# Performance work log

Hardware: AMD Instinct MI355X
Metric: run time of the kernel (lower is better)

Reference implementation:

```python
import jax, jax.numpy as jnp
import numpy as np

B, T, C = 4, 2048, 2048  # batch, n_target, n_context
KEY_SIZE = 1024
VALUE_SIZE = 1024
NUM_HEADS = 16
KEY_HIDDEN = 64
HEAD_SIZE = VALUE_SIZE // NUM_HEADS  # 64
NORMALISE = True


def setup_inputs() -> dict:
    key = jax.random.key(0)
    ks = jax.random.split(key, 7)
    s = 0.02
    return {
        "queries": jax.random.normal(ks[0], (B, T, KEY_SIZE), jnp.float32),
        "keys": jax.random.normal(ks[1], (B, C, KEY_SIZE), jnp.float32),
        "values": jax.random.normal(ks[2], (B, C, VALUE_SIZE), jnp.float32),
        "Wq": jax.random.normal(ks[3], (NUM_HEADS * KEY_HIDDEN, KEY_SIZE), jnp.float32) * s,
        "Wk": jax.random.normal(ks[4], (NUM_HEADS * KEY_HIDDEN, KEY_SIZE), jnp.float32) * s,
        "Wv": jax.random.normal(ks[5], (NUM_HEADS * HEAD_SIZE, VALUE_SIZE), jnp.float32) * s,
        "Wo": jax.random.normal(ks[6], (VALUE_SIZE, NUM_HEADS * HEAD_SIZE), jnp.float32) * s,
    }


def reference(queries, keys, values, Wq, Wk, Wv, Wo):
    # Linear projections (torch nn.Linear: x @ W.T), reshape to heads
    q = (queries @ Wq.T).reshape(B, T, NUM_HEADS, KEY_HIDDEN)   # [B,T,H,Dk]
    k = (keys @ Wk.T).reshape(B, C, NUM_HEADS, KEY_HIDDEN)      # [B,C,H,Dk]
    v = (values @ Wv.T).reshape(B, C, NUM_HEADS, HEAD_SIZE)     # [B,C,H,Dv]
    scale = np.sqrt(KEY_HIDDEN).astype(np.float32)
    # Scores [B,H,T,C]
    scores = jnp.einsum('bthd,bchd->bhtc', q, k) / scale
    if NORMALISE:
        attn = jax.nn.softmax(scores, axis=-1)
    else:
        attn = jax.nn.sigmoid(scores)
    out = jnp.einsum('bhtc,bchd->bthd', attn, v)                # [B,T,H,Dv]
    out = out.reshape(B, T, NUM_HEADS * HEAD_SIZE)
    return out @ Wo.T                                            # [B,T,VALUE_SIZE]
```

## Files before the change

### kernel.cpp

```cpp
#include <hip/hip_runtime.h>
#include <stdint.h>

#define BATCH 4
#define SEQ   2048
#define EMB   1024
#define NH    16
#define HD    64

typedef __attribute__((ext_vector_type(4))) float  floatx4;
typedef __attribute__((ext_vector_type(8))) short  shortx8;

__device__ __forceinline__ unsigned short f2bf(float f) {
  unsigned u = __builtin_bit_cast(unsigned, f);
  u += 0x7FFFu + ((u >> 16) & 1u);
  return (unsigned short)(u >> 16);
}

__device__ __forceinline__ unsigned pack2bf(float a, float b) {
  return (unsigned)f2bf(a) | ((unsigned)f2bf(b) << 16);
}

__device__ __forceinline__ unsigned packtrunc(float a, float b) {
#if __has_builtin(__builtin_amdgcn_perm)
  return __builtin_amdgcn_perm(__builtin_bit_cast(unsigned, b),
                               __builtin_bit_cast(unsigned, a), 0x07060302u);
#else
  return (__builtin_bit_cast(unsigned, a) >> 16) |
         (__builtin_bit_cast(unsigned, b) & 0xFFFF0000u);
#endif
}

__device__ __forceinline__ float fexp2(float x) {
#if __has_builtin(__builtin_amdgcn_exp2f)
  return __builtin_amdgcn_exp2f(x);
#else
  return exp2f(x);
#endif
}

__device__ __forceinline__ void gl_lds16(const void* g, void* l) {
  __builtin_amdgcn_global_load_lds((const __attribute__((address_space(1))) void*)g,
                                   (__attribute__((address_space(3))) void*)l,
                                   16, 0, 0);
}

__device__ __forceinline__ void cast_body(const float* __restrict__ in,
                                          unsigned short* __restrict__ out, int bb, int t) {
  size_t i = (size_t)bb * 256 + t;
  const float4* p = (const float4*)in + i * 2;
  float4 f0 = p[0], f1 = p[1];
  uint4 o;
  o.x = pack2bf(f0.x, f0.y);
  o.y = pack2bf(f0.z, f0.w);
  o.z = pack2bf(f1.x, f1.y);
  o.w = pack2bf(f1.z, f1.w);
  ((uint4*)out)[i] = o;
}

__global__ __launch_bounds__(256) void cast_bf16(const float* __restrict__ in,
                                                 unsigned short* __restrict__ out) {
  cast_body(in, out, blockIdx.x, threadIdx.x);
}

__global__ __launch_bounds__(256) void cast_all(
    const float* __restrict__ q, const float* __restrict__ k, const float* __restrict__ v,
    const float* __restrict__ w0, const float* __restrict__ w1,
    const float* __restrict__ w2, const float* __restrict__ w3,
    unsigned short* __restrict__ oq, unsigned short* __restrict__ ok, unsigned short* __restrict__ ov,
    unsigned short* __restrict__ ow0, unsigned short* __restrict__ ow1,
    unsigned short* __restrict__ ow2, unsigned short* __restrict__ ow3) {
  int bb = blockIdx.x;
  const float* in; unsigned short* out;
  if      (bb < 4096)  { in = q;  out = oq; }
  else if (bb < 8192)  { in = k;  out = ok;  bb -= 4096; }
  else if (bb < 12288) { in = v;  out = ov;  bb -= 8192; }
  else if (bb < 12800) { in = w0; out = ow0; bb -= 12288; }
  else if (bb < 13312) { in = w1; out = ow1; bb -= 12800; }
  else if (bb < 13824) { in = w2; out = ow2; bb -= 13312; }
  else                 { in = w3; out = ow3; bb -= 13824; }
  cast_body(in, out, bb, threadIdx.x);
}

__global__ __launch_bounds__(256) void cast_w4(const float* __restrict__ i0, const float* __restrict__ i1,
                                               const float* __restrict__ i2, const float* __restrict__ i3,
                                               unsigned short* __restrict__ o0, unsigned short* __restrict__ o1,
                                               unsigned short* __restrict__ o2, unsigned short* __restrict__ o3) {
  int bb = blockIdx.x;
  const float* in; unsigned short* out;
  if      (bb < 512)  { in = i0; out = o0; }
  else if (bb < 1024) { in = i1; out = o1; bb -= 512; }
  else if (bb < 1536) { in = i2; out = o2; bb -= 1024; }
  else                { in = i3; out = o3; bb -= 1536; }
  cast_body(in, out, bb, threadIdx.x);
}

#define TST 136
template <int MODE>
__device__ __forceinline__ void gemm_body(const unsigned short* __restrict__ A,
                                          const unsigned short* __restrict__ Bt,
                                          void* __restrict__ Cp, float cscale,
                                          unsigned short* As, unsigned short* Bs,
                                          unsigned short* Ts) {
  constexpr int N = EMB, K = EMB;
  constexpr int BM = 128, BN = 128, BK = 64;
  const int t = threadIdx.x, w = t >> 6, lane = t & 63;
  const int quad = lane >> 4, lrow = lane & 15;
  const int m0 = blockIdx.y * BM, n0 = blockIdx.x * BN;
  const int wm = (w >> 1) * 64, wn = (w & 1) * 64;
  floatx4 acc[4][4] = {};

  const unsigned short* asrc[4];
  const unsigned short* bsrc[4];
#pragma unroll
  for (int i = 0; i < 4; i++) {
    int q = i * 256 + t;
    int r = q >> 3, kc = (q & 7) ^ (r & 7);
    asrc[i] = A + (size_t)(m0 + r) * K + kc * 8;
    bsrc[i] = Bt + (size_t)(n0 + r) * K + kc * 8;
  }

  for (int k0 = 0; k0 < K; k0 += BK) {
#pragma unroll
    for (int i = 0; i < 4; i++) {
      gl_lds16(asrc[i], (char*)As + (size_t)(i * 256 + w * 64) * 16);
      gl_lds16(bsrc[i], (char*)Bs + (size_t)(i * 256 + w * 64) * 16);
      asrc[i] += BK; bsrc[i] += BK;
    }
    __syncthreads();
#pragma unroll
    for (int ks = 0; ks < 2; ks++) {
      shortx8 a[4];
#pragma unroll
      for (int mi = 0; mi < 4; mi++) {
        int row = wm + mi * 16 + lrow;
        a[mi] = *(const shortx8*)(As + row * 64 + (((ks * 4 + quad) ^ (row & 7)) * 8));
      }
#pragma unroll
      for (int ni = 0; ni < 4; ni++) {
        int rowb = wn + ni * 16 + lrow;
        shortx8 b = *(const shortx8*)(Bs + rowb * 64 + (((ks * 4 + quad) ^ (rowb & 7)) * 8));
#pragma unroll
        for (int mi = 0; mi < 4; mi++)
          acc[mi][ni] = __builtin_amdgcn_mfma_f32_16x16x32_bf16(a[mi], b, acc[mi][ni], 0, 0, 0);
      }
    }
    __syncthreads();
  }

  if constexpr (MODE == 2) {
#pragma unroll
    for (int u = 0; u < 2; u++)
#pragma unroll
      for (int ni = 0; ni < 4; ni++) {
        uint4 p;
        p.x = pack2bf(acc[2 * u][ni][0], acc[2 * u + 1][ni][0]);
        p.y = pack2bf(acc[2 * u][ni][1], acc[2 * u + 1][ni][1]);
        p.z = pack2bf(acc[2 * u][ni][2], acc[2 * u + 1][ni][2]);
        p.w = pack2bf(acc[2 * u][ni][3], acc[2 * u + 1][ni][3]);
        int col = wn + ni * 16 + lrow;
        int cloc = wm + u * 32 + quad * 8;
        *(uint4*)(Ts + col * TST + cloc) = p;
      }
    __syncthreads();
    unsigned short* vTout = (unsigned short*)Cp;
    const int b = m0 >> 11, cbase = m0 & 2047, h0 = n0 >> 6;
#pragma unroll
    for (int i = 0; i < 8; i++) {
      int g = t + 256 * i;
      int hh2 = g >> 10, d = (g >> 4) & 63, a = g & 15;
      uint4 v = *(const uint4*)(Ts + (hh2 * 64 + d) * TST + a * 8);
      *(uint4*)(vTout + ((size_t)((b * NH + h0 + hh2) * HD + d)) * SEQ + cbase + a * 8) = v;
    }
    __syncthreads();
  } else {
#pragma unroll
    for (int mi = 0; mi < 4; mi++)
#pragma unroll
      for (int ni = 0; ni < 4; ni++)
#pragma unroll
        for (int r = 0; r < 4; r++) {
          int row = m0 + wm + mi * 16 + quad * 4 + r;
          int col = n0 + wn + ni * 16 + lrow;
          float v = acc[mi][ni][r] * cscale;
          if constexpr (MODE == 1) ((float*)Cp)[(size_t)row * N + col] = v;
          else                     ((unsigned short*)Cp)[(size_t)row * N + col] = f2bf(v);
        }
  }
}

__global__ __launch_bounds__(256, 2) void gemm_qk(
    const unsigned short* __restrict__ Xq, const unsigned short* __restrict__ Xk,
    const unsigned short* __restrict__ Wq, const unsigned short* __restrict__ Wk,
    unsigned short* __restrict__ Oq, unsigned short* __restrict__ Ok, float sq) {
  __shared__ unsigned short As[128 * 64];
  __shared__ unsigned short Bs[128 * 64];
  if (blockIdx.z == 0) gemm_body<0>(Xq, Wq, Oq, sq,   As, Bs, nullptr);
  else                 gemm_body<0>(Xk, Wk, Ok, 1.0f, As, Bs, nullptr);
}

__global__ __launch_bounds__(256, 2) void gemm_b(const unsigned short* __restrict__ A,
                                                 const unsigned short* __restrict__ Bt,
                                                 unsigned short* __restrict__ C, float sc) {
  __shared__ unsigned short As[128 * 64];
  __shared__ unsigned short Bs[128 * 64];
  gemm_body<0>(A, Bt, C, sc, As, Bs, nullptr);
}
__global__ __launch_bounds__(256, 2) void gemm_vt(const unsigned short* __restrict__ A,
                                                  const unsigned short* __restrict__ Bt,
                                                  unsigned short* __restrict__ C) {
  __shared__ unsigned short As[128 * 64];
  __shared__ unsigned short Bs[128 * 64];
  __shared__ unsigned short Ts[128 * TST];
  gemm_body<2>(A, Bt, C, 1.0f, As, Bs, Ts);
}
__global__ __launch_bounds__(256, 2) void gemm_o(const unsigned short* __restrict__ A,
                                                 const unsigned short* __restrict__ Bt,
                                                 float* __restrict__ C) {
  __shared__ unsigned short As[128 * 64];
  __shared__ unsigned short Bs[128 * 64];
  gemm_body<1>(A, Bt, C, 1.0f, As, Bs, nullptr);
}

__global__ __launch_bounds__(256, 2) void flash_attn(const unsigned short* __restrict__ qp,
                                                     const unsigned short* __restrict__ kp,
                                                     const unsigned short* __restrict__ vT,
                                                     unsigned short* __restrict__ ao) {
  __shared__ unsigned short Ks[2][64 * 64];
  __shared__ unsigned short Vts[2][64 * 64];
  __shared__ unsigned short Ps[4][16 * 40];
  const int h = blockIdx.x & (NH - 1), b = blockIdx.x >> 4;
  const int t0 = blockIdx.y * 256;
  const int t = threadIdx.x, w = t >> 6, lane = t & 63;
  const int quad = lane >> 4, lrow = lane & 15;

  shortx8 qfrag[2][4];
#pragma unroll
  for (int kk = 0; kk < 2; kk++)
#pragma unroll
    for (int mi = 0; mi < 4; mi++) {
      int row = w * 64 + mi * 16 + lrow;
      qfrag[kk][mi] = *(const shortx8*)(qp + ((size_t)(b * SEQ + t0 + row)) * EMB +
                                        h * HD + kk * 32 + quad * 8);
    }

  const unsigned short* ksrc[2];
  const unsigned short* vsrc[2];
#pragma unroll
  for (int i = 0; i < 2; i++) {
    int p = i * 256 + t;
    int r = p >> 3, kc = (p & 7) ^ (r & 7);
    ksrc[i] = kp + ((size_t)(b * SEQ + r)) * EMB + h * HD + kc * 8;
    vsrc[i] = vT + ((size_t)((b * NH + h) * HD + r)) * SEQ + kc * 8;
  }

  float l_st[4][4] = {};
  floatx4 accO[4][4] = {};

#pragma unroll
  for (int i = 0; i < 2; i++) {
    gl_lds16(ksrc[i], (char*)Ks[0] + (size_t)(i * 256 + w * 64) * 16);
    gl_lds16(vsrc[i], (char*)Vts[0] + (size_t)(i * 256 + w * 64) * 16);
    ksrc[i] += 64 * EMB;
    vsrc[i] += 64;
  }
  __syncthreads();

  for (int it = 0; it < SEQ / 64; ++it) {
    const int cur = it & 1;
    const unsigned short* Kc = Ks[cur];
    const unsigned short* Vc = Vts[cur];

    if (it + 1 < SEQ / 64) {
#pragma unroll
      for (int i = 0; i < 2; i++) {
        gl_lds16(ksrc[i], (char*)Ks[cur ^ 1] + (size_t)(i * 256 + w * 64) * 16);
        gl_lds16(vsrc[i], (char*)Vts[cur ^ 1] + (size_t)(i * 256 + w * 64) * 16);
        ksrc[i] += 64 * EMB;
        vsrc[i] += 64;
      }
    }

    floatx4 accS[4][4] = {};
    __builtin_amdgcn_s_setprio(1);
#pragma unroll
    for (int kk = 0; kk < 2; kk++) {
      int qk = quad + kk * 4;
#pragma unroll
      for (int ni = 0; ni < 4; ni++) {
        int rowb = ni * 16 + lrow;
        shortx8 bfr = *(const shortx8*)(Kc + rowb * 64 + ((qk ^ (rowb & 7)) * 8));
#pragma unroll
        for (int mi = 0; mi < 4; mi++)
          accS[mi][ni] = __builtin_amdgcn_mfma_f32_16x16x32_bf16(qfrag[kk][mi], bfr, accS[mi][ni], 0, 0, 0);
      }
    }
    __builtin_amdgcn_s_setprio(0);

#pragma unroll
    for (int hh = 0; hh < 2; hh++) {
      shortx8 pafr[4];
#pragma unroll
      for (int mi = 0; mi < 4; mi++) {
#pragma unroll
        for (int r = 0; r < 4; r++) {
          float p0 = fexp2(accS[mi][2 * hh][r]);
          float p1 = fexp2(accS[mi][2 * hh + 1][r]);
          l_st[mi][r] += p0 + p1;
          *(unsigned*)(&Ps[w][(quad * 4 + r) * 40 + lrow * 2]) = packtrunc(p0, p1);
        }
        pafr[mi] = *(const shortx8*)(&Ps[w][lrow * 40 + quad * 8]);
      }
      __builtin_amdgcn_s_setprio(1);
#pragma unroll
      for (int nio = 0; nio < 4; nio++) {
        int d = nio * 16 + lrow;
        shortx8 bfr = *(const shortx8*)(Vc + d * 64 + ((((hh << 2) + quad) ^ (d & 7)) * 8));
#pragma unroll
        for (int mi = 0; mi < 4; mi++)
          accO[mi][nio] = __builtin_amdgcn_mfma_f32_16x16x32_bf16(pafr[mi], bfr, accO[mi][nio], 0, 0, 0);
      }
      __builtin_amdgcn_s_setprio(0);
    }

    __syncthreads();
  }

#pragma unroll
  for (int mi = 0; mi < 4; mi++)
#pragma unroll
    for (int r = 0; r < 4; r++) {
      float l = l_st[mi][r];
      l += __shfl_xor(l, 1);
      l += __shfl_xor(l, 2);
      l += __shfl_xor(l, 4);
      l += __shfl_xor(l, 8);
      float inv = 1.0f / l;
#pragma unroll
      for (int nio = 0; nio < 4; nio++) accO[mi][nio][r] *= inv;
    }
#pragma unroll
  for (int mi = 0; mi < 4; mi++)
#pragma unroll
    for (int nio = 0; nio < 4; nio++)
#pragma unroll
      for (int r = 0; r < 4; r++) {
        int row = t0 + w * 64 + mi * 16 + quad * 4 + r;
        int col = h * HD + nio * 16 + lrow;
        ao[((size_t)(b * SEQ + row)) * EMB + col] = f2bf(accO[mi][nio][r]);
      }
}

extern "C" void kernel_launch(void* const* d_in, const int* in_sizes, int n_in,
                              void* d_out, int out_size, void* d_ws, size_t ws_size,
                              hipStream_t stream) {
  const float* queries = (const float*)d_in[0];
  const float* keys    = (const float*)d_in[1];
  const float* values  = (const float*)d_in[2];
  const float* Wq      = (const float*)d_in[3];
  const float* Wk      = (const float*)d_in[4];
  const float* Wv      = (const float*)d_in[5];
  const float* Wo      = (const float*)d_in[6];

  char* ws = (char*)d_ws;
  const size_t MB = 1ull << 20;
  const float SC2 = 0.125f * 1.44269504088896341f;

  unsigned short* wq_b = (unsigned short*)(ws + 0 * MB);
  unsigned short* wk_b = (unsigned short*)(ws + 2 * MB);
  unsigned short* wv_b = (unsigned short*)(ws + 4 * MB);
  unsigned short* wo_b = (unsigned short*)(ws + 6 * MB);

  dim3 gg(EMB / 128, (BATCH * SEQ) / 128);
  dim3 fg(NH * BATCH, SEQ / 256);

  if (ws_size >= 104 * MB) {
    unsigned short* Xq = (unsigned short*)(ws + 8 * MB);
    unsigned short* Xk = (unsigned short*)(ws + 24 * MB);
    unsigned short* Xv = (unsigned short*)(ws + 40 * MB);
    unsigned short* qp = (unsigned short*)(ws + 56 * MB);
    unsigned short* kp = (unsigned short*)(ws + 72 * MB);
    unsigned short* vT = (unsigned short*)(ws + 88 * MB);
    unsigned short* ao = Xq;

    cast_all<<<14336, 256, 0, stream>>>(queries, keys, values, Wq, Wk, Wv, Wo,
                                        Xq, Xk, Xv, wq_b, wk_b, wv_b, wo_b);
    gemm_qk<<<dim3(gg.x, gg.y, 2), 256, 0, stream>>>(Xq, Xk, wq_b, wk_b, qp, kp, SC2);
    gemm_vt<<<gg, 256, 0, stream>>>(Xv, wv_b, vT);
    flash_attn<<<fg, 256, 0, stream>>>(qp, kp, vT, ao);
    gemm_o<<<gg, 256, 0, stream>>>(ao, wo_b, (float*)d_out);
  } else {
    unsigned short* X  = (unsigned short*)(ws + 8 * MB);
    unsigned short* qp = (unsigned short*)(ws + 24 * MB);
    unsigned short* kp = (unsigned short*)(ws + 40 * MB);
    unsigned short* vT = (unsigned short*)(ws + 56 * MB);
    unsigned short* ao = X;

    cast_w4<<<2048, 256, 0, stream>>>(Wq, Wk, Wv, Wo, wq_b, wk_b, wv_b, wo_b);
    cast_bf16<<<4096, 256, 0, stream>>>(queries, X);
    gemm_b<<<gg, 256, 0, stream>>>(X, wq_b, qp, SC2);
    cast_bf16<<<4096, 256, 0, stream>>>(keys, X);
    gemm_b<<<gg, 256, 0, stream>>>(X, wk_b, kp, 1.0f);
    cast_bf16<<<4096, 256, 0, stream>>>(values, X);
    gemm_vt<<<gg, 256, 0, stream>>>(X, wv_b, vT);
    flash_attn<<<fg, 256, 0, stream>>>(qp, kp, vT, ao);
    gemm_o<<<gg, 256, 0, stream>>>(ao, wo_b, (float*)d_out);
  }
}
```

Measured before the change: 328.8 us.

## Fuse fp32-to-bf16 activation cast into projection GEMM A-tile loads

Removes the separate activation cast kernels and the bf16 intermediate buffers. The Q/K/V projection GEMMs now read fp32 activations directly into registers, convert them to bf16 and write them to swizzled LDS, while weights still use async global-to-LDS loads. This drops a full write and read of the 3x32MB activations, at the cost of synchronous register-staged A loads that lose the async LDS path and raise register pressure. Each N-tile column block rereads the fp32 A rows, which doubles A traffic per GEMM compared with the bf16 copies.

```diff
diff --git a/kernel.cpp b/kernel.cpp
--- a/kernel.cpp
+++ b/kernel.cpp
@@ -57,30 +57,6 @@
   ((uint4*)out)[i] = o;
 }
 
-__global__ __launch_bounds__(256) void cast_bf16(const float* __restrict__ in,
-                                                 unsigned short* __restrict__ out) {
-  cast_body(in, out, blockIdx.x, threadIdx.x);
-}
-
-__global__ __launch_bounds__(256) void cast_all(
-    const float* __restrict__ q, const float* __restrict__ k, const float* __restrict__ v,
-    const float* __restrict__ w0, const float* __restrict__ w1,
-    const float* __restrict__ w2, const float* __restrict__ w3,
-    unsigned short* __restrict__ oq, unsigned short* __restrict__ ok, unsigned short* __restrict__ ov,
-    unsigned short* __restrict__ ow0, unsigned short* __restrict__ ow1,
-    unsigned short* __restrict__ ow2, unsigned short* __restrict__ ow3) {
-  int bb = blockIdx.x;
-  const float* in; unsigned short* out;
-  if      (bb < 4096)  { in = q;  out = oq; }
-  else if (bb < 8192)  { in = k;  out = ok;  bb -= 4096; }
-  else if (bb < 12288) { in = v;  out = ov;  bb -= 8192; }
-  else if (bb < 12800) { in = w0; out = ow0; bb -= 12288; }
-  else if (bb < 13312) { in = w1; out = ow1; bb -= 12800; }
-  else if (bb < 13824) { in = w2; out = ow2; bb -= 13312; }
-  else                 { in = w3; out = ow3; bb -= 13824; }
-  cast_body(in, out, bb, threadIdx.x);
-}
-
 __global__ __launch_bounds__(256) void cast_w4(const float* __restrict__ i0, const float* __restrict__ i1,
                                                const float* __restrict__ i2, const float* __restrict__ i3,
                                                unsigned short* __restrict__ o0, unsigned short* __restrict__ o1,
@@ -95,8 +71,8 @@
 }
 
 #define TST 136
-template <int MODE>
-__device__ __forceinline__ void gemm_body(const unsigned short* __restrict__ A,
+template <int MODE, bool CASTA>
+__device__ __forceinline__ void gemm_body(const void* __restrict__ Ap,
                                           const unsigned short* __restrict__ Bt,
                                           void* __restrict__ Cp, float cscale,
                                           unsigned short* As, unsigned short* Bs,
@@ -110,21 +86,53 @@
   floatx4 acc[4][4] = {};
 
   const unsigned short* asrc[4];
+  const float*          afsrc[4];
+  int                   adst[4];
   const unsigned short* bsrc[4];
 #pragma unroll
   for (int i = 0; i < 4; i++) {
     int q = i * 256 + t;
-    int r = q >> 3, kc = (q & 7) ^ (r & 7);
-    asrc[i] = A + (size_t)(m0 + r) * K + kc * 8;
+    int r = q >> 3, kc0 = q & 7, kc = kc0 ^ (r & 7);
+    if constexpr (CASTA) {
+      afsrc[i] = (const float*)Ap + (size_t)(m0 + r) * K + kc0 * 8;
+      adst[i] = r * 64 + kc * 8;
+    } else {
+      asrc[i] = (const unsigned short*)Ap + (size_t)(m0 + r) * K + kc * 8;
+    }
     bsrc[i] = Bt + (size_t)(n0 + r) * K + kc * 8;
   }
 
   for (int k0 = 0; k0 < K; k0 += BK) {
-#pragma unroll
-    for (int i = 0; i < 4; i++) {
-      gl_lds16(asrc[i], (char*)As + (size_t)(i * 256 + w * 64) * 16);
-      gl_lds16(bsrc[i], (char*)Bs + (size_t)(i * 256 + w * 64) * 16);
-      asrc[i] += BK; bsrc[i] += BK;
+    if constexpr (CASTA) {
+      float4 fa[4][2];
+#pragma unroll
+      for (int i = 0; i < 4; i++) {
+        const float4* s = (const float4*)afsrc[i];
+        fa[i][0] = s[0];
+        fa[i][1] = s[1];
+        afsrc[i] += BK;
+      }
+#pragma unroll
+      for (int i = 0; i < 4; i++) {
+        gl_lds16(bsrc[i], (char*)Bs + (size_t)(i * 256 + w * 64) * 16);
+        bsrc[i] += BK;
+      }
+#pragma unroll
+      for (int i = 0; i < 4; i++) {
+        uint4 o;
+        o.x = pack2bf(fa[i][0].x, fa[i][0].y);
+        o.y = pack2bf(fa[i][0].z, fa[i][0].w);
+        o.z = pack2bf(fa[i][1].x, fa[i][1].y);
+        o.w = pack2bf(fa[i][1].z, fa[i][1].w);
+        *(uint4*)(As + adst[i]) = o;
+      }
+    } else {
+#pragma unroll
+      for (int i = 0; i < 4; i++) {
+        gl_lds16(asrc[i], (char*)As + (size_t)(i * 256 + w * 64) * 16);
+        gl_lds16(bsrc[i], (char*)Bs + (size_t)(i * 256 + w * 64) * 16);
+        asrc[i] += BK; bsrc[i] += BK;
+      }
     }
     __syncthreads();
 #pragma unroll
@@ -188,37 +196,31 @@
   }
 }
 
-__global__ __launch_bounds__(256, 2) void gemm_qk(
-    const unsigned short* __restrict__ Xq, const unsigned short* __restrict__ Xk,
+__global__ __launch_bounds__(256, 2) void gemm_qkf(
+    const float* __restrict__ Xq, const float* __restrict__ Xk,
     const unsigned short* __restrict__ Wq, const unsigned short* __restrict__ Wk,
     unsigned short* __restrict__ Oq, unsigned short* __restrict__ Ok, float sq) {
   __shared__ unsigned short As[128 * 64];
   __shared__ unsigned short Bs[128 * 64];
-  if (blockIdx.z == 0) gemm_body<0>(Xq, Wq, Oq, sq,   As, Bs, nullptr);
-  else                 gemm_body<0>(Xk, Wk, Ok, 1.0f, As, Bs, nullptr);
-}
-
-__global__ __launch_bounds__(256, 2) void gemm_b(const unsigned short* __restrict__ A,
-                                                 const unsigned short* __restrict__ Bt,
-                                                 unsigned short* __restrict__ C, float sc) {
-  __shared__ unsigned short As[128 * 64];
-  __shared__ unsigned short Bs[128 * 64];
-  gemm_body<0>(A, Bt, C, sc, As, Bs, nullptr);
-}
-__global__ __launch_bounds__(256, 2) void gemm_vt(const unsigned short* __restrict__ A,
-                                                  const unsigned short* __restrict__ Bt,
-                                                  unsigned short* __restrict__ C) {
+  if (blockIdx.z == 0) gemm_body<0, true>(Xq, Wq, Oq, sq,   As, Bs, nullptr);
+  else                 gemm_body<0, true>(Xk, Wk, Ok, 1.0f, As, Bs, nullptr);
+}
+
+__global__ __launch_bounds__(256, 2) void gemm_vtf(const float* __restrict__ Xv,
+                                                   const unsigned short* __restrict__ Wv,
+                                                   unsigned short* __restrict__ vT) {
   __shared__ unsigned short As[128 * 64];
   __shared__ unsigned short Bs[128 * 64];
   __shared__ unsigned short Ts[128 * TST];
-  gemm_body<2>(A, Bt, C, 1.0f, As, Bs, Ts);
-}
+  gemm_body<2, true>(Xv, Wv, vT, 1.0f, As, Bs, Ts);
+}
+
 __global__ __launch_bounds__(256, 2) void gemm_o(const unsigned short* __restrict__ A,
                                                  const unsigned short* __restrict__ Bt,
                                                  float* __restrict__ C) {
   __shared__ unsigned short As[128 * 64];
   __shared__ unsigned short Bs[128 * 64];
-  gemm_body<1>(A, Bt, C, 1.0f, As, Bs, nullptr);
+  gemm_body<1, false>(A, Bt, C, 1.0f, As, Bs, nullptr);
 }
 
 __global__ __launch_bounds__(256, 2) void flash_attn(const unsigned short* __restrict__ qp,
@@ -369,40 +371,17 @@
   unsigned short* wk_b = (unsigned short*)(ws + 2 * MB);
   unsigned short* wv_b = (unsigned short*)(ws + 4 * MB);
   unsigned short* wo_b = (unsigned short*)(ws + 6 * MB);
+  unsigned short* ao   = (unsigned short*)(ws + 8 * MB);
+  unsigned short* qp   = (unsigned short*)(ws + 24 * MB);
+  unsigned short* kp   = (unsigned short*)(ws + 40 * MB);
+  unsigned short* vT   = (unsigned short*)(ws + 56 * MB);
 
   dim3 gg(EMB / 128, (BATCH * SEQ) / 128);
   dim3 fg(NH * BATCH, SEQ / 256);
 
-  if (ws_size >= 104 * MB) {
-    unsigned short* Xq = (unsigned short*)(ws + 8 * MB);
-    unsigned short* Xk = (unsigned short*)(ws + 24 * MB);
-    unsigned short* Xv = (unsigned short*)(ws + 40 * MB);
-    unsigned short* qp = (unsigned short*)(ws + 56 * MB);
-    unsigned short* kp = (unsigned short*)(ws + 72 * MB);
-    unsigned short* vT = (unsigned short*)(ws + 88 * MB);
-    unsigned short* ao = Xq;
-
-    cast_all<<<14336, 256, 0, stream>>>(queries, keys, values, Wq, Wk, Wv, Wo,
-                                        Xq, Xk, Xv, wq_b, wk_b, wv_b, wo_b);
-    gemm_qk<<<dim3(gg.x, gg.y, 2), 256, 0, stream>>>(Xq, Xk, wq_b, wk_b, qp, kp, SC2);
-    gemm_vt<<<gg, 256, 0, stream>>>(Xv, wv_b, vT);
-    flash_attn<<<fg, 256, 0, stream>>>(qp, kp, vT, ao);
-    gemm_o<<<gg, 256, 0, stream>>>(ao, wo_b, (float*)d_out);
-  } else {
-    unsigned short* X  = (unsigned short*)(ws + 8 * MB);
-    unsigned short* qp = (unsigned short*)(ws + 24 * MB);
-    unsigned short* kp = (unsigned short*)(ws + 40 * MB);
-    unsigned short* vT = (unsigned short*)(ws + 56 * MB);
-    unsigned short* ao = X;
-
-    cast_w4<<<2048, 256, 0, stream>>>(Wq, Wk, Wv, Wo, wq_b, wk_b, wv_b, wo_b);
-    cast_bf16<<<4096, 256, 0, stream>>>(queries, X);
-    gemm_b<<<gg, 256, 0, stream>>>(X, wq_b, qp, SC2);
-    cast_bf16<<<4096, 256, 0, stream>>>(keys, X);
-    gemm_b<<<gg, 256, 0, stream>>>(X, wk_b, kp, 1.0f);
-    cast_bf16<<<4096, 256, 0, stream>>>(values, X);
-    gemm_vt<<<gg, 256, 0, stream>>>(X, wv_b, vT);
-    flash_attn<<<fg, 256, 0, stream>>>(qp, kp, vT, ao);
-    gemm_o<<<gg, 256, 0, stream>>>(ao, wo_b, (float*)d_out);
-  }
-}
+  cast_w4<<<2048, 256, 0, stream>>>(Wq, Wk, Wv, Wo, wq_b, wk_b, wv_b, wo_b);
+  gemm_qkf<<<dim3(gg.x, gg.y, 2), 256, 0, stream>>>(queries, keys, wq_b, wk_b, qp, kp, SC2);
+  gemm_vtf<<<gg, 256, 0, stream>>>(values, wv_b, vT);
+  flash_attn<<<fg, 256, 0, stream>>>(qp, kp, vT, ao);
+  gemm_o<<<gg, 256, 0, stream>>>(ao, wo_b, (float*)d_out);
+}
```

Measured after the change: 361.3 us. +9.9%, slower.
